# Optimization experiments

Measured on AMD Instinct MI355X. Metric: run time of the kernel, lower is better.

Reference implementation:

```python
import jax, jax.numpy as jnp
import numpy as np

B, IN_DIM, SIZE = 1024, 64, 2048
D1, D2 = 64, 64  # hidden_dims=[64], out_dim=64 (depth=2, linspace default)
NEG_SLOPE = 0.2


def setup_inputs() -> dict:
    key = jax.random.key(0)
    ks = jax.random.split(key, 5)
    x = jax.random.normal(ks[0], (B, IN_DIM), dtype=jnp.float32)
    # conv_0: Conv1d(1, size*d1, kernel=in_dim) weight (size*d1, 1, in_dim) -> (size, d1, in_dim)
    W0 = jax.random.normal(ks[1], (SIZE, D1, IN_DIM), dtype=jnp.float32) * (1.0 / np.sqrt(IN_DIM))
    b0 = jax.random.normal(ks[2], (SIZE, D1), dtype=jnp.float32) * 0.01
    # conv_1: Conv1d(size, size*d2, kernel=d1, groups=size) weight (size*d2, 1, d1) -> (size, d2, d1)
    W1 = jax.random.normal(ks[3], (SIZE, D2, D1), dtype=jnp.float32) * (1.0 / np.sqrt(D1))
    b1 = jax.random.normal(ks[4], (SIZE, D2), dtype=jnp.float32) * 0.01
    return {"x": x, "W0": W0, "b0": b0, "W1": W1, "b1": b1}


def reference(x, W0, b0, W1, b1):
    # Layer 0: full-length Conv1d over 1 input channel == dense linear broadcast over groups.
    # h[b,g,j] = sum_k W0[g,j,k] * x[b,k] + b0[g,j]
    h = jnp.einsum('bk,gjk->bgj', x, W0) + b0  # (B, SIZE, D1)
    h = jnp.where(h > 0, h, NEG_SLOPE * h)     # LeakyReLU(0.2)
    # Layer 1: grouped full-length Conv1d == independent per-group linear maps.
    # out[b,g,j] = sum_k W1[g,j,k] * h[b,g,k] + b1[g,j]
    out = jnp.einsum('bgk,gjk->bgj', h, W1) + b1  # (B, SIZE, D2)
    return out
```

## Files before the change

### kernel.cpp

```cpp
#include <hip/hip_runtime.h>

#define BATCH 1024
#define NGRP  2048
#define DIM   64
#define MT    128
#define LDR   68

typedef __attribute__((ext_vector_type(8)))  short bf16x8;
typedef __attribute__((ext_vector_type(4)))  short short4v;
typedef __attribute__((ext_vector_type(16))) float f32x16;

__device__ __forceinline__ short f2bf(float f) {
    union { float f; unsigned u; } v; v.f = f;
    unsigned r = v.u + 0x7fffu + ((v.u >> 16) & 1u);
    return (short)(r >> 16);
}

__global__ __launch_bounds__(256, 2)
void convnn_kernel(const float* __restrict__ x,  const float* __restrict__ W0,
                   const float* __restrict__ b0, const float* __restrict__ W1,
                   const float* __restrict__ b1, float* __restrict__ out) {
    __shared__ short xs[MT][LDR];
    __shared__ short hs[MT][LDR];
    __shared__ short w0s[DIM][LDR];
    __shared__ short w1s[DIM][LDR];
    __shared__ float b0s[DIM], b1s[DIM];

    const int g     = blockIdx.x >> 3;
    const int mbase = (blockIdx.x & 7) * MT;
    const int tid   = threadIdx.x;

    {
        const float* xp = x + (size_t)mbase * DIM;
        #pragma unroll
        for (int i = 0; i < 8; ++i) {
            int f   = tid + i * 256;
            int row = f >> 4;
            int c   = (f & 15) * 4;
            float4 v = *(const float4*)(xp + row * DIM + c);
            short4v s = { f2bf(v.x), f2bf(v.y), f2bf(v.z), f2bf(v.w) };
            *(short4v*)&xs[row][c] = s;
        }
        const float* w0p = W0 + (size_t)g * DIM * DIM;
        const float* w1p = W1 + (size_t)g * DIM * DIM;
        #pragma unroll
        for (int i = 0; i < 4; ++i) {
            int f   = tid + i * 256;
            int row = f >> 4;
            int c   = (f & 15) * 4;
            float4 v0 = *(const float4*)(w0p + row * DIM + c);
            short4v s0 = { f2bf(v0.x), f2bf(v0.y), f2bf(v0.z), f2bf(v0.w) };
            *(short4v*)&w0s[row][c] = s0;
            float4 v1 = *(const float4*)(w1p + row * DIM + c);
            short4v s1 = { f2bf(v1.x), f2bf(v1.y), f2bf(v1.z), f2bf(v1.w) };
            *(short4v*)&w1s[row][c] = s1;
        }
        if (tid < DIM)          b0s[tid]       = b0[(size_t)g * DIM + tid];
        else if (tid < 2 * DIM) b1s[tid - DIM] = b1[(size_t)g * DIM + tid - DIM];
    }
    __syncthreads();

    const int lane = tid & 63;
    const int wave = tid >> 6;
    const int lm   = lane & 31;
    const int koff = (lane >> 5) * 8;
    const int mw   = wave * 32;

    f32x16 acc0, acc1;
    #pragma unroll
    for (int i = 0; i < 16; ++i) { acc0[i] = 0.f; acc1[i] = 0.f; }
    #pragma unroll
    for (int kk = 0; kk < 4; ++kk) {
        int k = kk * 16 + koff;
        bf16x8 a, bA, bB;
        a.lo  = *(const short4v*)&xs[mw + lm][k];
        a.hi  = *(const short4v*)&xs[mw + lm][k + 4];
        bA.lo = *(const short4v*)&w0s[lm][k];
        bA.hi = *(const short4v*)&w0s[lm][k + 4];
        bB.lo = *(const short4v*)&w0s[32 + lm][k];
        bB.hi = *(const short4v*)&w0s[32 + lm][k + 4];
        acc0 = __builtin_amdgcn_mfma_f32_32x32x16_bf16(a, bA, acc0, 0, 0, 0);
        acc1 = __builtin_amdgcn_mfma_f32_32x32x16_bf16(a, bB, acc1, 0, 0, 0);
    }
    #pragma unroll
    for (int r = 0; r < 16; ++r) {
        int row = mw + (r & 3) + 8 * (r >> 2) + 4 * (lane >> 5);
        float v0 = acc0[r] + b0s[lm];
        v0 = v0 > 0.f ? v0 : 0.2f * v0;
        hs[row][lm] = f2bf(v0);
        float v1 = acc1[r] + b0s[32 + lm];
        v1 = v1 > 0.f ? v1 : 0.2f * v1;
        hs[row][32 + lm] = f2bf(v1);
    }
    __syncthreads();

    f32x16 c0, c1;
    #pragma unroll
    for (int i = 0; i < 16; ++i) { c0[i] = 0.f; c1[i] = 0.f; }
    #pragma unroll
    for (int kk = 0; kk < 4; ++kk) {
        int k = kk * 16 + koff;
        bf16x8 a, bA, bB;
        a.lo  = *(const short4v*)&hs[mw + lm][k];
        a.hi  = *(const short4v*)&hs[mw + lm][k + 4];
        bA.lo = *(const short4v*)&w1s[lm][k];
        bA.hi = *(const short4v*)&w1s[lm][k + 4];
        bB.lo = *(const short4v*)&w1s[32 + lm][k];
        bB.hi = *(const short4v*)&w1s[32 + lm][k + 4];
        c0 = __builtin_amdgcn_mfma_f32_32x32x16_bf16(a, bA, c0, 0, 0, 0);
        c1 = __builtin_amdgcn_mfma_f32_32x32x16_bf16(a, bB, c1, 0, 0, 0);
    }
    #pragma unroll
    for (int r = 0; r < 16; ++r) {
        int row  = (r & 3) + 8 * (r >> 2) + 4 * (lane >> 5);
        size_t b = (size_t)(mbase + mw + row);
        float* o = out + b * ((size_t)NGRP * DIM) + (size_t)g * DIM;
        o[lm]      = c0[r] + b1s[lm];
        o[32 + lm] = c1[r] + b1s[32 + lm];
    }
}

extern "C" void kernel_launch(void* const* d_in, const int* in_sizes, int n_in,
                              void* d_out, int out_size, void* d_ws, size_t ws_size,
                              hipStream_t stream) {
    const float* x  = (const float*)d_in[0];
    const float* W0 = (const float*)d_in[1];
    const float* b0 = (const float*)d_in[2];
    const float* W1 = (const float*)d_in[3];
    const float* b1 = (const float*)d_in[4];
    float* out = (float*)d_out;
    dim3 grid(NGRP * (BATCH / MT));
    convnn_kernel<<<grid, dim3(256), 0, stream>>>(x, W0, b0, W1, b1, out);
}
```

Before: 660.9 us.

## Keep per-group weights in registers, loop over batch, pre-convert x to bf16

Launches one block per group instead of eight, so W0/W1 are loaded and converted to bf16 once per group and kept in registers as MFMA fragments across eight batch tiles per wave. A small pre-kernel converts x to bf16 in the workspace, and each wave prefetches its next x tile from global memory while computing. Column pairs are interleaved so outputs are written as float2, and LDS use drops to one per-wave h tile with no block-wide barriers. This targets repeated weight loading, conversion work and barrier cost, in exchange for higher register pressure, an extra launch and fewer blocks.

```diff
diff --git a/kernel.cpp b/kernel.cpp
--- a/kernel.cpp
+++ b/kernel.cpp
@@ -3,120 +3,133 @@
 #define BATCH 1024
 #define NGRP  2048
 #define DIM   64
-#define MT    128
-#define LDR   68
+#define NEG   0.2f
+#define OUTSTRIDE ((size_t)NGRP * DIM)
 
 typedef __attribute__((ext_vector_type(8)))  short bf16x8;
 typedef __attribute__((ext_vector_type(4)))  short short4v;
 typedef __attribute__((ext_vector_type(16))) float f32x16;
 
-__device__ __forceinline__ short f2bf(float f) {
-    union { float f; unsigned u; } v; v.f = f;
-    unsigned r = v.u + 0x7fffu + ((v.u >> 16) & 1u);
-    return (short)(r >> 16);
+union frag_u { bf16x8 v; unsigned u[4]; short4v h[2]; };
+
+__device__ __forceinline__ unsigned pk_rne(float a, float b) {
+    unsigned ua = __float_as_uint(a), ub = __float_as_uint(b);
+    ua += 0x7fffu + ((ua >> 16) & 1u);
+    ub += 0x7fffu + ((ub >> 16) & 1u);
+    return __builtin_amdgcn_perm(ub, ua, 0x07060302);
 }
 
-__global__ __launch_bounds__(256, 2)
-void convnn_kernel(const float* __restrict__ x,  const float* __restrict__ W0,
-                   const float* __restrict__ b0, const float* __restrict__ W1,
-                   const float* __restrict__ b1, float* __restrict__ out) {
-    __shared__ short xs[MT][LDR];
-    __shared__ short hs[MT][LDR];
-    __shared__ short w0s[DIM][LDR];
-    __shared__ short w1s[DIM][LDR];
-    __shared__ float b0s[DIM], b1s[DIM];
+__global__ void cvt_x_kernel(const float4* __restrict__ x, uint2* __restrict__ xb) {
+    int i = blockIdx.x * blockDim.x + threadIdx.x;
+    float4 v = x[i];
+    uint2 o;
+    o.x = pk_rne(v.x, v.y);
+    o.y = pk_rne(v.z, v.w);
+    xb[i] = o;
+}
 
-    const int g     = blockIdx.x >> 3;
-    const int mbase = (blockIdx.x & 7) * MT;
-    const int tid   = threadIdx.x;
+__global__ __launch_bounds__(256, 3)
+void convnn_kernel(const unsigned short* __restrict__ xb,
+                   const float* __restrict__ W0, const float* __restrict__ b0,
+                   const float* __restrict__ W1, const float* __restrict__ b1,
+                   float* __restrict__ out) {
+    __shared__ short hs[4][32][68];
 
+    const int g    = blockIdx.x;
+    const int tid  = threadIdx.x;
+    const int lane = tid & 63;
+    const int wave = tid >> 6;
+    const int n    = lane & 31;
+    const int koff = (lane >> 5) * 8;
+
+    frag_u w0f[4][2], w1f[4][2];
     {
-        const float* xp = x + (size_t)mbase * DIM;
-        #pragma unroll
-        for (int i = 0; i < 8; ++i) {
-            int f   = tid + i * 256;
-            int row = f >> 4;
-            int c   = (f & 15) * 4;
-            float4 v = *(const float4*)(xp + row * DIM + c);
-            short4v s = { f2bf(v.x), f2bf(v.y), f2bf(v.z), f2bf(v.w) };
-            *(short4v*)&xs[row][c] = s;
-        }
         const float* w0p = W0 + (size_t)g * DIM * DIM;
         const float* w1p = W1 + (size_t)g * DIM * DIM;
         #pragma unroll
-        for (int i = 0; i < 4; ++i) {
-            int f   = tid + i * 256;
-            int row = f >> 4;
-            int c   = (f & 15) * 4;
-            float4 v0 = *(const float4*)(w0p + row * DIM + c);
-            short4v s0 = { f2bf(v0.x), f2bf(v0.y), f2bf(v0.z), f2bf(v0.w) };
-            *(short4v*)&w0s[row][c] = s0;
-            float4 v1 = *(const float4*)(w1p + row * DIM + c);
-            short4v s1 = { f2bf(v1.x), f2bf(v1.y), f2bf(v1.z), f2bf(v1.w) };
-            *(short4v*)&w1s[row][c] = s1;
+        for (int kk = 0; kk < 4; ++kk) {
+            #pragma unroll
+            for (int p = 0; p < 2; ++p) {
+                const float* r0 = w0p + (size_t)(2 * n + p) * DIM + kk * 16 + koff;
+                float4 lo = *(const float4*)r0;
+                float4 hi = *(const float4*)(r0 + 4);
+                w0f[kk][p].u[0] = pk_rne(lo.x, lo.y);
+                w0f[kk][p].u[1] = pk_rne(lo.z, lo.w);
+                w0f[kk][p].u[2] = pk_rne(hi.x, hi.y);
+                w0f[kk][p].u[3] = pk_rne(hi.z, hi.w);
+                const float* r1 = w1p + (size_t)(2 * n + p) * DIM + kk * 16 + koff;
+                float4 lo1 = *(const float4*)r1;
+                float4 hi1 = *(const float4*)(r1 + 4);
+                w1f[kk][p].u[0] = pk_rne(lo1.x, lo1.y);
+                w1f[kk][p].u[1] = pk_rne(lo1.z, lo1.w);
+                w1f[kk][p].u[2] = pk_rne(hi1.x, hi1.y);
+                w1f[kk][p].u[3] = pk_rne(hi1.z, hi1.w);
+            }
         }
-        if (tid < DIM)          b0s[tid]       = b0[(size_t)g * DIM + tid];
-        else if (tid < 2 * DIM) b1s[tid - DIM] = b1[(size_t)g * DIM + tid - DIM];
     }
-    __syncthreads();
+    const float2 b0v = *(const float2*)(b0 + (size_t)g * DIM + 2 * n);
+    const float2 b1v = *(const float2*)(b1 + (size_t)g * DIM + 2 * n);
 
-    const int lane = tid & 63;
-    const int wave = tid >> 6;
-    const int lm   = lane & 31;
-    const int koff = (lane >> 5) * 8;
-    const int mw   = wave * 32;
+    short (*h)[68] = hs[wave];
 
-    f32x16 acc0, acc1;
-    #pragma unroll
-    for (int i = 0; i < 16; ++i) { acc0[i] = 0.f; acc1[i] = 0.f; }
-    #pragma unroll
-    for (int kk = 0; kk < 4; ++kk) {
-        int k = kk * 16 + koff;
-        bf16x8 a, bA, bB;
-        a.lo  = *(const short4v*)&xs[mw + lm][k];
-        a.hi  = *(const short4v*)&xs[mw + lm][k + 4];
-        bA.lo = *(const short4v*)&w0s[lm][k];
-        bA.hi = *(const short4v*)&w0s[lm][k + 4];
-        bB.lo = *(const short4v*)&w0s[32 + lm][k];
-        bB.hi = *(const short4v*)&w0s[32 + lm][k + 4];
-        acc0 = __builtin_amdgcn_mfma_f32_32x32x16_bf16(a, bA, acc0, 0, 0, 0);
-        acc1 = __builtin_amdgcn_mfma_f32_32x32x16_bf16(a, bB, acc1, 0, 0, 0);
+    bf16x8 a[4];
+    {
+        int tb = wave * 32;
+        const unsigned short* xr = xb + (size_t)(tb + n) * DIM + koff;
+        #pragma unroll
+        for (int kk = 0; kk < 4; ++kk) a[kk] = *(const bf16x8*)(xr + kk * 16);
     }
-    #pragma unroll
-    for (int r = 0; r < 16; ++r) {
-        int row = mw + (r & 3) + 8 * (r >> 2) + 4 * (lane >> 5);
-        float v0 = acc0[r] + b0s[lm];
-        v0 = v0 > 0.f ? v0 : 0.2f * v0;
-        hs[row][lm] = f2bf(v0);
-        float v1 = acc1[r] + b0s[32 + lm];
-        v1 = v1 > 0.f ? v1 : 0.2f * v1;
-        hs[row][32 + lm] = f2bf(v1);
-    }
-    __syncthreads();
 
-    f32x16 c0, c1;
-    #pragma unroll
-    for (int i = 0; i < 16; ++i) { c0[i] = 0.f; c1[i] = 0.f; }
-    #pragma unroll
-    for (int kk = 0; kk < 4; ++kk) {
-        int k = kk * 16 + koff;
-        bf16x8 a, bA, bB;
-        a.lo  = *(const short4v*)&hs[mw + lm][k];
-        a.hi  = *(const short4v*)&hs[mw + lm][k + 4];
-        bA.lo = *(const short4v*)&w1s[lm][k];
-        bA.hi = *(const short4v*)&w1s[lm][k + 4];
-        bB.lo = *(const short4v*)&w1s[32 + lm][k];
-        bB.hi = *(const short4v*)&w1s[32 + lm][k + 4];
-        c0 = __builtin_amdgcn_mfma_f32_32x32x16_bf16(a, bA, c0, 0, 0, 0);
-        c1 = __builtin_amdgcn_mfma_f32_32x32x16_bf16(a, bB, c1, 0, 0, 0);
-    }
-    #pragma unroll
-    for (int r = 0; r < 16; ++r) {
-        int row  = (r & 3) + 8 * (r >> 2) + 4 * (lane >> 5);
-        size_t b = (size_t)(mbase + mw + row);
-        float* o = out + b * ((size_t)NGRP * DIM) + (size_t)g * DIM;
-        o[lm]      = c0[r] + b1s[lm];
-        o[32 + lm] = c1[r] + b1s[32 + lm];
+    for (int i = 0; i < 8; ++i) {
+        const int tb = (i * 4 + wave) * 32;
+        bf16x8 an[4];
+        {
+            int tn = ((i < 7 ? i + 1 : 7) * 4 + wave) * 32;
+            const unsigned short* xr = xb + (size_t)(tn + n) * DIM + koff;
+            #pragma unroll
+            for (int kk = 0; kk < 4; ++kk) an[kk] = *(const bf16x8*)(xr + kk * 16);
+        }
+
+        f32x16 aE, aO;
+        #pragma unroll
+        for (int r = 0; r < 16; ++r) { aE[r] = 0.f; aO[r] = 0.f; }
+        #pragma unroll
+        for (int kk = 0; kk < 4; ++kk) {
+            aE = __builtin_amdgcn_mfma_f32_32x32x16_bf16(a[kk], w0f[kk][0].v, aE, 0, 0, 0);
+            aO = __builtin_amdgcn_mfma_f32_32x32x16_bf16(a[kk], w0f[kk][1].v, aO, 0, 0, 0);
+        }
+        #pragma unroll
+        for (int r = 0; r < 16; ++r) {
+            int m = (r & 3) + 8 * (r >> 2) + 4 * (lane >> 5);
+            float vE = aE[r] + b0v.x; vE = vE > 0.f ? vE : NEG * vE;
+            float vO = aO[r] + b0v.y; vO = vO > 0.f ? vO : NEG * vO;
+            *(unsigned*)&h[m][2 * n] = pk_rne(vE, vO);
+        }
+
+        f32x16 cE, cO;
+        #pragma unroll
+        for (int r = 0; r < 16; ++r) { cE[r] = 0.f; cO[r] = 0.f; }
+        #pragma unroll
+        for (int kk = 0; kk < 4; ++kk) {
+            frag_u hf;
+            hf.h[0] = *(const short4v*)&h[n][kk * 16 + koff];
+            hf.h[1] = *(const short4v*)&h[n][kk * 16 + koff + 4];
+            cE = __builtin_amdgcn_mfma_f32_32x32x16_bf16(hf.v, w1f[kk][0].v, cE, 0, 0, 0);
+            cO = __builtin_amdgcn_mfma_f32_32x32x16_bf16(hf.v, w1f[kk][1].v, cO, 0, 0, 0);
+        }
+
+        float* ob = out + (size_t)tb * OUTSTRIDE + (size_t)g * DIM + 2 * n;
+        #pragma unroll
+        for (int r = 0; r < 16; ++r) {
+            int m = (r & 3) + 8 * (r >> 2) + 4 * (lane >> 5);
+            float2 o2;
+            o2.x = cE[r] + b1v.x;
+            o2.y = cO[r] + b1v.y;
+            *(float2*)(ob + (size_t)m * OUTSTRIDE) = o2;
+        }
+
+        #pragma unroll
+        for (int kk = 0; kk < 4; ++kk) a[kk] = an[kk];
     }
 }
 
@@ -129,6 +142,8 @@
     const float* W1 = (const float*)d_in[3];
     const float* b1 = (const float*)d_in[4];
     float* out = (float*)d_out;
-    dim3 grid(NGRP * (BATCH / MT));
-    convnn_kernel<<<grid, dim3(256), 0, stream>>>(x, W0, b0, W1, b1, out);
+    unsigned short* xb = (unsigned short*)d_ws;
+
+    cvt_x_kernel<<<dim3(64), dim3(256), 0, stream>>>((const float4*)x, (uint2*)xb);
+    convnn_kernel<<<dim3(NGRP), dim3(256), 0, stream>>>(xb, W0, b0, W1, b1, out);
 }
```

Result: faster. 606.8 us (-8.2%).
